# Performance work log

Hardware: AMD Instinct MI355X
Metric: run time of the kernel (lower is better)

Reference implementation:

```python
import math
import jax, jax.numpy as jnp
import numpy as np

HIDDEN = 2048
N_HEADS = 16
N_KV_HEADS = 4
HEAD_DIM = HIDDEN // N_HEADS  # 128
SEQ = 2048
BATCH = 2
RMS_EPS = 1.1920928955078125e-07  # torch float32 eps (nn.RMSNorm default eps=None)


def setup_inputs() -> dict:
    key = jax.random.key(0)
    ks = jax.random.split(key, 8)
    x = jax.random.normal(ks[0], (BATCH, SEQ, HIDDEN), dtype=jnp.float32)
    # RoPE tables, half-rotation layout: [f0..f_{d/2-1}, f0..f_{d/2-1}]
    inv_freq = 1.0 / (10000.0 ** (jnp.arange(0, HEAD_DIM, 2, dtype=jnp.float32) / HEAD_DIM))
    t = jnp.arange(SEQ, dtype=jnp.float32)
    freqs = jnp.outer(t, inv_freq)                      # [S, D/2]
    emb = jnp.concatenate([freqs, freqs], axis=-1)      # [S, D]
    sin, cos = jnp.sin(emb), jnp.cos(emb)
    s = 0.02
    Wq = jax.random.normal(ks[1], (HIDDEN, HIDDEN), dtype=jnp.float32) * s
    Wk = jax.random.normal(ks[2], (HIDDEN, N_KV_HEADS * HEAD_DIM), dtype=jnp.float32) * s
    Wv = jax.random.normal(ks[3], (HIDDEN, N_KV_HEADS * HEAD_DIM), dtype=jnp.float32) * s
    Wo = jax.random.normal(ks[4], (HIDDEN, HIDDEN), dtype=jnp.float32) * s
    q_norm_w = jnp.ones((HEAD_DIM,), dtype=jnp.float32)
    k_norm_w = jnp.ones((HEAD_DIM,), dtype=jnp.float32)
    return {"x": x, "sin": sin, "cos": cos, "Wq": Wq, "Wk": Wk, "Wv": Wv,
            "Wo": Wo, "q_norm_w": q_norm_w, "k_norm_w": k_norm_w}


def _rms_norm(t, w):
    # RMSNorm over last dim (head_dim) with learned weight
    var = jnp.mean(t * t, axis=-1, keepdims=True)
    return t * jax.lax.rsqrt(var + RMS_EPS) * w


def _apply_rope(t, sin, cos):
    # t: [B, H, S, D]; sin/cos: [S, D] broadcast
    half = t.shape[-1] // 2
    rotated = jnp.concatenate([-t[..., half:], t[..., :half]], axis=-1)
    return cos * t + sin * rotated


def reference(x, sin, cos, Wq, Wk, Wv, Wo, q_norm_w, k_norm_w):
    b, s, _ = x.shape
    rep = N_HEADS // N_KV_HEADS
    # Q: proj -> norm -> transpose -> rope
    q = (x @ Wq).reshape(b, s, N_HEADS, HEAD_DIM)
    q = _rms_norm(q, q_norm_w).transpose(0, 2, 1, 3)           # [B, H, S, D]
    q = _apply_rope(q, sin, cos)
    # K: proj -> repeat kv heads -> norm -> transpose -> rope
    k = (x @ Wk).reshape(b, s, N_KV_HEADS, HEAD_DIM)
    k = jnp.repeat(k, rep, axis=2)                              # [B, S, H, D]
    k = _rms_norm(k, k_norm_w).transpose(0, 2, 1, 3)            # [B, H, S, D]
    k = _apply_rope(k, sin, cos)
    # V: proj -> repeat kv heads -> transpose
    v = (x @ Wv).reshape(b, s, N_KV_HEADS, HEAD_DIM)
    v = jnp.repeat(v, rep, axis=2).transpose(0, 2, 1, 3)        # [B, H, S, D]
    # explicit masked softmax attention (materializes [B,H,S,S])
    scores = jnp.einsum('bhqd,bhkd->bhqk', q, k) / math.sqrt(HEAD_DIM)
    causal = jnp.triu(jnp.ones((s, s), dtype=bool), 1)
    scores = jnp.where(causal, -jnp.inf, scores)
    attn = jax.nn.softmax(scores, axis=-1)
    o = jnp.einsum('bhqk,bhkd->bhqd', attn, v)                  # [B, H, S, D]
    o = o.transpose(0, 2, 1, 3).reshape(b, s, HIDDEN)
    return o @ Wo
```

## Files before the change

kernel.cpp:

```cpp
#include <hip/hip_runtime.h>

typedef __attribute__((ext_vector_type(8))) short bf16x8;
typedef __attribute__((ext_vector_type(4))) short bf16x4;
typedef __attribute__((ext_vector_type(4))) float f32x4;

#define HIDDEN 2048
#define NH 16
#define NKV 4
#define HD 128
#define SEQ_N 2048
#define NT 4096
#define QKV_N 3072
#define RMS_EPS 1.1920928955078125e-07f
#define QSCALE 0.08838834764831845f
#define SM_C 12.0f

static __device__ __forceinline__ float b2f(unsigned short u) {
  union { unsigned int i; float f; } v; v.i = ((unsigned int)u) << 16; return v.f;
}
static __device__ __forceinline__ unsigned short f2b(float f) {
  union { float f; unsigned int i; } v; v.f = f;
  unsigned int r = (v.i + 0x7fffu + ((v.i >> 16) & 1u)) >> 16;
  return (unsigned short)r;
}
static __device__ __forceinline__ void gload_lds16(const unsigned short* g, unsigned short* l) {
  __builtin_amdgcn_global_load_lds(
      (const __attribute__((address_space(1))) unsigned int*)g,
      (__attribute__((address_space(3))) unsigned int*)l, 16, 0, 0);
}
static __device__ __forceinline__ void store_c(float* p, float v) { *p = v; }
static __device__ __forceinline__ void store_c(unsigned short* p, float v) { *p = f2b(v); }

template <typename OutT>
__device__ __forceinline__ void gemm_tile(
    const unsigned short* __restrict__ A, int lda,
    const unsigned short* __restrict__ BT, int ldb,
    OutT* __restrict__ C, int ldc,
    int K, int m0, int nloc0, int nout0) {
  __shared__ unsigned short As[4096], Bs[4096];
  const int tid  = threadIdx.x;
  const int wid  = tid >> 6, lane = tid & 63;
  const int g    = lane >> 4, cc = lane & 15;
  const int wr   = wid >> 1,  wc = wid & 1;
  const int r0   = tid >> 2;
  const int cb0  = (tid & 3) * 8;

  f32x4 acc[4][4];
#pragma unroll
  for (int i = 0; i < 4; ++i)
#pragma unroll
    for (int j = 0; j < 4; ++j) acc[i][j] = (f32x4){0.f, 0.f, 0.f, 0.f};

  unsigned short* AsW0 = As + wid * 512;
  unsigned short* AsW1 = As + 2048 + wid * 512;
  unsigned short* BsW0 = Bs + wid * 512;
  unsigned short* BsW1 = Bs + 2048 + wid * 512;
  const unsigned short* Ab0 = A  + (size_t)(m0 + r0)        * lda + cb0;
  const unsigned short* Ab1 = A  + (size_t)(m0 + 64 + r0)   * lda + cb0;
  const unsigned short* Bb0 = BT + (size_t)(nloc0 + r0)     * ldb + cb0;
  const unsigned short* Bb1 = BT + (size_t)(nloc0 + 64 + r0)* ldb + cb0;

  for (int kt = 0; kt < K; kt += 32) {
    gload_lds16(Ab0 + kt, AsW0);
    gload_lds16(Ab1 + kt, AsW1);
    gload_lds16(Bb0 + kt, BsW0);
    gload_lds16(Bb1 + kt, BsW1);
    __syncthreads();
    bf16x8 af[4], bfr[4];
#pragma unroll
    for (int mi = 0; mi < 4; ++mi)
      af[mi] = *(const bf16x8*)(As + ((wr * 64 + mi * 16 + cc) * 32 + g * 8));
#pragma unroll
    for (int ni = 0; ni < 4; ++ni)
      bfr[ni] = *(const bf16x8*)(Bs + ((wc * 64 + ni * 16 + cc) * 32 + g * 8));
#pragma unroll
    for (int mi = 0; mi < 4; ++mi)
#pragma unroll
      for (int ni = 0; ni < 4; ++ni)
        acc[mi][ni] = __builtin_amdgcn_mfma_f32_16x16x32_bf16(af[mi], bfr[ni], acc[mi][ni], 0, 0, 0);
    __syncthreads();
  }
#pragma unroll
  for (int mi = 0; mi < 4; ++mi)
#pragma unroll
    for (int ni = 0; ni < 4; ++ni)
#pragma unroll
      for (int j = 0; j < 4; ++j) {
        int row = m0 + wr * 64 + mi * 16 + g * 4 + j;
        int col = nout0 + wc * 64 + ni * 16 + cc;
        store_c(&C[(size_t)row * ldc + col], acc[mi][ni][j]);
      }
}

__global__ __launch_bounds__(256) void k_gemm_qkv(
    const unsigned short* __restrict__ x,
    const unsigned short* __restrict__ WqT,
    const unsigned short* __restrict__ WkT,
    const unsigned short* __restrict__ WvT,
    unsigned short* __restrict__ Praw) {
  int wg = (blockIdx.x & 7) * 96 + (blockIdx.x >> 3);
  int nb = wg % 24, mb = wg / 24;
  int n0 = nb * 128;
  const unsigned short* BT; int nloc;
  if (n0 < HIDDEN)            { BT = WqT; nloc = n0; }
  else if (n0 < HIDDEN + 512) { BT = WkT; nloc = n0 - HIDDEN; }
  else                        { BT = WvT; nloc = n0 - (HIDDEN + 512); }
  gemm_tile<unsigned short>(x, HIDDEN, BT, HIDDEN, Praw, QKV_N, HIDDEN, mb * 128, nloc, n0);
}

__global__ __launch_bounds__(256) void k_gemm_o(
    const unsigned short* __restrict__ Oa,
    const unsigned short* __restrict__ WoT,
    float* __restrict__ out) {
  int wg = (blockIdx.x & 7) * 64 + (blockIdx.x >> 3);
  int nb = wg % 16, mb = wg / 16;
  gemm_tile<float>(Oa, HIDDEN, WoT, HIDDEN, out, HIDDEN, HIDDEN, mb * 128, nb * 128, nb * 128);
}

__global__ __launch_bounds__(256) void k_cvt_f2b(
    const float* __restrict__ src, unsigned short* __restrict__ dst) {
  int i = (blockIdx.x * 256 + threadIdx.x) * 8;
  float4 a = *(const float4*)(src + i);
  float4 b = *(const float4*)(src + i + 4);
  bf16x8 v;
  v[0] = (short)f2b(a.x); v[1] = (short)f2b(a.y); v[2] = (short)f2b(a.z); v[3] = (short)f2b(a.w);
  v[4] = (short)f2b(b.x); v[5] = (short)f2b(b.y); v[6] = (short)f2b(b.z); v[7] = (short)f2b(b.w);
  *(bf16x8*)(dst + i) = v;
}

__global__ __launch_bounds__(256) void k_transpose_f2b(
    const float* __restrict__ src, unsigned short* __restrict__ dst,
    int ld_src, int ld_dst, int tilesC) {
  __shared__ float T[64][68];
  int tr = blockIdx.x / tilesC, tc = blockIdx.x % tilesC;
  int r0 = tr * 64, c0 = tc * 64;
  int tid = threadIdx.x;
#pragma unroll
  for (int it = 0; it < 4; ++it) {
    int u = it * 256 + tid;
    int r = u >> 4, cb = (u & 15) * 4;
    float4 v = *(const float4*)(src + (size_t)(r0 + r) * ld_src + c0 + cb);
    T[r][cb] = v.x; T[r][cb + 1] = v.y; T[r][cb + 2] = v.z; T[r][cb + 3] = v.w;
  }
  __syncthreads();
#pragma unroll
  for (int it = 0; it < 2; ++it) {
    int u = it * 256 + tid;
    int dc = u >> 3, rb = (u & 7) * 8;
    bf16x8 v;
#pragma unroll
    for (int j = 0; j < 8; ++j) v[j] = (short)f2b(T[rb + j][dc]);
    *(bf16x8*)(dst + (size_t)(c0 + dc) * ld_dst + r0 + rb) = v;
  }
}

__global__ __launch_bounds__(256) void k_transpose_bb(
    const unsigned short* __restrict__ src, unsigned short* __restrict__ dst,
    int ld_src, int ld_dst, int tilesC) {
  __shared__ unsigned short T[64][80];
  int tr = blockIdx.x / tilesC, tc = blockIdx.x % tilesC;
  int r0 = tr * 64, c0 = tc * 64;
  int tid = threadIdx.x;
#pragma unroll
  for (int it = 0; it < 2; ++it) {
    int u = it * 256 + tid; int r = u >> 3, cb = (u & 7) * 8;
    bf16x8 v = *(const bf16x8*)(src + (size_t)(r0 + r) * ld_src + c0 + cb);
    *(bf16x8*)(&T[r][cb]) = v;
  }
  __syncthreads();
#pragma unroll
  for (int it = 0; it < 2; ++it) {
    int u = it * 256 + tid; int dc = u >> 3, rb = (u & 7) * 8;
    bf16x8 v;
#pragma unroll
    for (int j = 0; j < 8; ++j) v[j] = (short)T[rb + j][dc];
    *(bf16x8*)(dst + (size_t)(c0 + dc) * ld_dst + r0 + rb) = v;
  }
}

__global__ __launch_bounds__(256) void k_qk_post(
    const unsigned short* __restrict__ Praw,
    const float* __restrict__ sinT,
    const float* __restrict__ cosT,
    const float* __restrict__ qw,
    const float* __restrict__ kw,
    unsigned short* __restrict__ Qbuf,
    unsigned short* __restrict__ Kbuf) {
  int sub = threadIdx.x >> 4;
  int sl  = threadIdx.x & 15;
  int rid = blockIdx.x * 16 + sub;
  int t = rid / 20, slot = rid - t * 20;
  int b = t >> 11, s = t & 2047;
  const int isq = (slot < 16);
  int cb = isq ? slot * 128 : HIDDEN + (slot - 16) * 128;
  const unsigned short* src = Praw + (size_t)t * QKV_N + cb;
  const int d0 = sl * 4;
  bf16x4 a0 = *(const bf16x4*)(src + d0);
  bf16x4 a1 = *(const bf16x4*)(src + 64 + d0);
  float x0[4], x1[4];
  float ssq = 0.f;
#pragma unroll
  for (int j = 0; j < 4; ++j) {
    x0[j] = b2f((unsigned short)a0[j]);
    x1[j] = b2f((unsigned short)a1[j]);
    ssq += x0[j] * x0[j] + x1[j] * x1[j];
  }
#pragma unroll
  for (int mk = 1; mk < 16; mk <<= 1) ssq += __shfl_xor(ssq, mk, 64);
  float r = rsqrtf(ssq * (1.0f / 128.0f) + RMS_EPS);
  const float* w = isq ? qw : kw;
  f32x4 w0 = *(const f32x4*)(w + d0);
  f32x4 w1 = *(const f32x4*)(w + 64 + d0);
  f32x4 cs0 = *(const f32x4*)(cosT + s * 128 + d0);
  f32x4 cs1 = *(const f32x4*)(cosT + s * 128 + 64 + d0);
  f32x4 sn0 = *(const f32x4*)(sinT + s * 128 + d0);
  f32x4 sn1 = *(const f32x4*)(sinT + s * 128 + 64 + d0);
  unsigned short* dst = isq
      ? Qbuf + ((size_t)(b * NH + slot) * SEQ_N + s) * HD
      : Kbuf + ((size_t)(b * NKV + (slot - 16)) * SEQ_N + s) * HD;
  const float qs = isq ? QSCALE : 1.0f;
  bf16x4 o0, o1;
#pragma unroll
  for (int j = 0; j < 4; ++j) {
    float n0 = x0[j] * r * w0[j];
    float n1 = x1[j] * r * w1[j];
    o0[j] = (short)f2b((cs0[j] * n0 - sn0[j] * n1) * qs);
    o1[j] = (short)f2b((cs1[j] * n1 + sn1[j] * n0) * qs);
  }
  *(bf16x4*)(dst + d0) = o0;
  *(bf16x4*)(dst + 64 + d0) = o1;
}

__global__ __launch_bounds__(256, 2) void k_attn(
    const unsigned short* __restrict__ Q,
    const unsigned short* __restrict__ K,
    const unsigned short* __restrict__ V,
    unsigned short* __restrict__ O) {
  __shared__ unsigned short Ks[2][64 * 128];
  __shared__ unsigned short Vs[2][128 * 64];
  __shared__ unsigned short Ps[4][16 * 64];
  const int tid = threadIdx.x, wid = tid >> 6, lane = tid & 63;
  const int g = lane >> 4, c = lane & 15;
  const int bid = blockIdx.x;
  const int bh = bid & 31;
  const int b = bh >> 4, h = bh & 15;
  const int z = bid >> 5;
  const int zz = z & 7, zr = z >> 3;
  const int qt = (zr == 0) ? zz : (zr == 1) ? 15 - zz : (zr == 2) ? 16 + zz : 31 - zz;
  const int wq0 = qt * 64 + wid * 16;
  const int kv = h >> 2;
  const int nt = qt + 1;

  const unsigned short* Qp = Q + (size_t)(b * NH + h) * SEQ_N * HD;
  const unsigned short* Kp = K + (size_t)(b * NKV + kv) * SEQ_N * HD;
  const unsigned short* Vp = V + (size_t)(kv * HD) * NT + b * SEQ_N;

  const int krow_l = lane >> 4;
  const int kcol_l = (lane & 15) * 8;
  const int vrow_l = lane >> 3;
  const int vcol_l = (lane & 7) * 8;

  bf16x8 qfr[4];
#pragma unroll
  for (int ks = 0; ks < 4; ++ks)
    qfr[ks] = *(const bf16x8*)(Qp + (size_t)(wq0 + c) * HD + ks * 32 + g * 8);

  f32x4 o[8];
#pragma unroll
  for (int df = 0; df < 8; ++df) o[df] = (f32x4){0.f, 0.f, 0.f, 0.f};
  float l_i[4] = {0.f, 0.f, 0.f, 0.f};

#define STAGE(BUF, KBASE)                                                          \
  {                                                                                \
    _Pragma("unroll")                                                              \
    for (int ch = 0; ch < 4; ++ch) {                                               \
      int chunk = wid * 4 + ch;                                                    \
      int rk = chunk * 4 + krow_l;                                                 \
      int ck = kcol_l ^ ((rk & 15) << 3);                                          \
      gload_lds16(Kp + (size_t)((KBASE) + rk) * HD + ck, &Ks[BUF][chunk * 512]);   \
      int rv = chunk * 8 + vrow_l;                                                 \
      int cv = vcol_l ^ ((rv & 7) << 3);                                           \
      gload_lds16(Vp + (size_t)rv * NT + (KBASE) + cv, &Vs[BUF][chunk * 512]);     \
    }                                                                              \
  }

  int buf = 0;
  STAGE(0, 0);
  __syncthreads();

  for (int kt = 0; kt < nt; ++kt) {
    const int kbase = kt * 64;
    if (kt + 1 < nt) STAGE(buf ^ 1, kbase + 64);

    f32x4 s[4];
#pragma unroll
    for (int kf = 0; kf < 4; ++kf) s[kf] = (f32x4){0.f, 0.f, 0.f, 0.f};
    __builtin_amdgcn_s_setprio(1);
#pragma unroll
    for (int ks = 0; ks < 4; ++ks) {
      bf16x8 bk[4];
#pragma unroll
      for (int kf = 0; kf < 4; ++kf) {
        int r = kf * 16 + c;
        int e = (ks * 32 + g * 8) ^ ((r & 15) << 3);
        bk[kf] = *(const bf16x8*)(&Ks[buf][r * 128 + e]);
      }
#pragma unroll
      for (int kf = 0; kf < 4; ++kf)
        s[kf] = __builtin_amdgcn_mfma_f32_16x16x32_bf16(qfr[ks], bk[kf], s[kf], 0, 0, 0);
    }
    __builtin_amdgcn_s_setprio(0);
    if (kbase + 63 > wq0) {
#pragma unroll
      for (int kf = 0; kf < 4; ++kf)
#pragma unroll
        for (int i = 0; i < 4; ++i) {
          int q = wq0 + g * 4 + i;
          int kp = kbase + kf * 16 + c;
          if (kp > q) s[kf][i] = -1e30f;
        }
    }
#pragma unroll
    for (int kf = 0; kf < 4; ++kf)
#pragma unroll
      for (int i = 0; i < 4; ++i) {
        float p = __expf(s[kf][i] - SM_C);
        l_i[i] += p;
        int r = g * 4 + i;
        int e = (kf * 16 + c) ^ ((r & 7) << 3);
        Ps[wid][r * 64 + e] = f2b(p);
      }
    __builtin_amdgcn_s_setprio(1);
#pragma unroll
    for (int ksp = 0; ksp < 2; ++ksp) {
      int ep = (ksp * 32 + g * 8) ^ ((c & 7) << 3);
      bf16x8 pa = *(const bf16x8*)(&Ps[wid][c * 64 + ep]);
#pragma unroll
      for (int df = 0; df < 8; ++df) {
        int rv = df * 16 + c;
        int e = (ksp * 32 + g * 8) ^ ((rv & 7) << 3);
        bf16x8 vb = *(const bf16x8*)(&Vs[buf][rv * 64 + e]);
        o[df] = __builtin_amdgcn_mfma_f32_16x16x32_bf16(pa, vb, o[df], 0, 0, 0);
      }
    }
    __builtin_amdgcn_s_setprio(0);
    __syncthreads();
    buf ^= 1;
  }

  unsigned short* Op = O + (size_t)(b * SEQ_N) * HIDDEN + h * HD;
#pragma unroll
  for (int i = 0; i < 4; ++i) {
    float t = l_i[i];
    t += __shfl_xor(t, 1, 64);
    t += __shfl_xor(t, 2, 64);
    t += __shfl_xor(t, 4, 64);
    t += __shfl_xor(t, 8, 64);
    float inv = 1.0f / t;
    int q = wq0 + g * 4 + i;
#pragma unroll
    for (int df = 0; df < 8; ++df)
      Op[(size_t)q * HIDDEN + df * 16 + c] = f2b(o[df][i] * inv);
  }
#undef STAGE
}

extern "C" void kernel_launch(void* const* d_in, const int* in_sizes, int n_in,
                              void* d_out, int out_size, void* d_ws, size_t ws_size,
                              hipStream_t stream) {
  const float* x    = (const float*)d_in[0];
  const float* sinT = (const float*)d_in[1];
  const float* cosT = (const float*)d_in[2];
  const float* Wq   = (const float*)d_in[3];
  const float* Wk   = (const float*)d_in[4];
  const float* Wv   = (const float*)d_in[5];
  const float* Wo   = (const float*)d_in[6];
  const float* qw   = (const float*)d_in[7];
  const float* kw   = (const float*)d_in[8];
  float* out = (float*)d_out;
  unsigned short* ws = (unsigned short*)d_ws;

  unsigned short* Xb   = ws;
  unsigned short* WqT  = ws + 8388608;
  unsigned short* WkT  = ws + 12582912;
  unsigned short* WvT  = ws + 13631488;
  unsigned short* WoT  = ws + 14680064;
  unsigned short* Praw = ws + 18874368;
  unsigned short* Qbuf = ws + 31457280;
  unsigned short* Kbuf = ws + 39845888;
  unsigned short* Vt   = ws + 41943040;
  unsigned short* Oatt = ws + 44040192;

  dim3 blk(256);
  k_cvt_f2b<<<4096, blk, 0, stream>>>(x, Xb);
  k_transpose_f2b<<<1024, blk, 0, stream>>>(Wq, WqT, 2048, 2048, 32);
  k_transpose_f2b<<<256,  blk, 0, stream>>>(Wk, WkT, 512,  2048, 8);
  k_transpose_f2b<<<256,  blk, 0, stream>>>(Wv, WvT, 512,  2048, 8);
  k_transpose_f2b<<<1024, blk, 0, stream>>>(Wo, WoT, 2048, 2048, 32);
  k_gemm_qkv<<<768, blk, 0, stream>>>(Xb, WqT, WkT, WvT, Praw);
  k_qk_post<<<5120, blk, 0, stream>>>(Praw, sinT, cosT, qw, kw, Qbuf, Kbuf);
  k_transpose_bb<<<512, blk, 0, stream>>>(Praw + 2560, Vt, 3072, 4096, 8);
  k_attn<<<1024, blk, 0, stream>>>(Qbuf, Kbuf, Vt, Oatt);
  k_gemm_o<<<512, blk, 0, stream>>>(Oatt, WoT, out);
}
```

Measured before the change: 321.0 us.

## Rewrite projection GEMMs with 128x256 tiles, double-buffered LDS and XOR swizzle

Replaces the single-buffered 128x128 GEMM tile (256 threads, K-step 32) with a 128x256 tile run by 512 threads that steps K by 64. The LDS is double-buffered so the next stage is prefetched while the current one is computed, using explicit vmcnt waits and raw barriers. Reads use an XOR swizzle to avoid bank conflicts, and MFMA sections are bracketed by s_setprio. This targets the per-iteration sync and load latency and raises data reuse, at the cost of much larger LDS use (96KB per block) and fewer blocks in the QKV and O GEMM grids.

```diff
diff --git a/kernel.cpp b/kernel.cpp
--- a/kernel.cpp
+++ b/kernel.cpp
@@ -32,18 +32,18 @@
 static __device__ __forceinline__ void store_c(unsigned short* p, float v) { *p = f2b(v); }
 
 template <typename OutT>
-__device__ __forceinline__ void gemm_tile(
+__device__ __forceinline__ void gemm8_tile(
     const unsigned short* __restrict__ A, int lda,
     const unsigned short* __restrict__ BT, int ldb,
     OutT* __restrict__ C, int ldc,
     int K, int m0, int nloc0, int nout0) {
-  __shared__ unsigned short As[4096], Bs[4096];
-  const int tid  = threadIdx.x;
-  const int wid  = tid >> 6, lane = tid & 63;
-  const int g    = lane >> 4, cc = lane & 15;
-  const int wr   = wid >> 1,  wc = wid & 1;
-  const int r0   = tid >> 2;
-  const int cb0  = (tid & 3) * 8;
+  __shared__ unsigned short As[2][128 * 64];
+  __shared__ unsigned short Bs[2][256 * 64];
+  const int tid = threadIdx.x;
+  const int wid = tid >> 6, lane = tid & 63;
+  const int g = lane >> 4, cc = lane & 15;
+  const int wr = wid >> 2, wc = wid & 3;
+  const int sr = lane >> 3, scb = lane & 7;
 
   f32x4 acc[4][4];
 #pragma unroll
@@ -51,35 +51,73 @@
 #pragma unroll
     for (int j = 0; j < 4; ++j) acc[i][j] = (f32x4){0.f, 0.f, 0.f, 0.f};
 
-  unsigned short* AsW0 = As + wid * 512;
-  unsigned short* AsW1 = As + 2048 + wid * 512;
-  unsigned short* BsW0 = Bs + wid * 512;
-  unsigned short* BsW1 = Bs + 2048 + wid * 512;
-  const unsigned short* Ab0 = A  + (size_t)(m0 + r0)        * lda + cb0;
-  const unsigned short* Ab1 = A  + (size_t)(m0 + 64 + r0)   * lda + cb0;
-  const unsigned short* Bb0 = BT + (size_t)(nloc0 + r0)     * ldb + cb0;
-  const unsigned short* Bb1 = BT + (size_t)(nloc0 + 64 + r0)* ldb + cb0;
-
-  for (int kt = 0; kt < K; kt += 32) {
-    gload_lds16(Ab0 + kt, AsW0);
-    gload_lds16(Ab1 + kt, AsW1);
-    gload_lds16(Bb0 + kt, BsW0);
-    gload_lds16(Bb1 + kt, BsW1);
-    __syncthreads();
-    bf16x8 af[4], bfr[4];
-#pragma unroll
-    for (int mi = 0; mi < 4; ++mi)
-      af[mi] = *(const bf16x8*)(As + ((wr * 64 + mi * 16 + cc) * 32 + g * 8));
+#define STAGE8(BUF, KT)                                                              \
+  {                                                                                  \
+    _Pragma("unroll")                                                                \
+    for (int i = 0; i < 2; ++i) {                                                    \
+      int r = i * 64 + wid * 8 + sr;                                                 \
+      gload_lds16(A + (size_t)(m0 + r) * lda + (KT) + ((scb ^ (r & 7)) << 3),        \
+                  &As[BUF][i * 4096 + wid * 512]);                                   \
+    }                                                                                \
+    _Pragma("unroll")                                                                \
+    for (int i = 0; i < 4; ++i) {                                                    \
+      int r = i * 64 + wid * 8 + sr;                                                 \
+      gload_lds16(BT + (size_t)(nloc0 + r) * ldb + (KT) + ((scb ^ (r & 7)) << 3),    \
+                  &Bs[BUF][i * 4096 + wid * 512]);                                   \
+    }                                                                                \
+  }
+
+  int buf = 0;
+  STAGE8(0, 0);
+  STAGE8(1, 64);
+  asm volatile("s_waitcnt vmcnt(6)" ::: "memory");
+  __builtin_amdgcn_s_barrier();
+  asm volatile("" ::: "memory");
+
+  for (int kt = 0; kt < K; kt += 64) {
+    bf16x8 bfr[4][2];
 #pragma unroll
     for (int ni = 0; ni < 4; ++ni)
-      bfr[ni] = *(const bf16x8*)(Bs + ((wc * 64 + ni * 16 + cc) * 32 + g * 8));
-#pragma unroll
-    for (int mi = 0; mi < 4; ++mi)
-#pragma unroll
-      for (int ni = 0; ni < 4; ++ni)
-        acc[mi][ni] = __builtin_amdgcn_mfma_f32_16x16x32_bf16(af[mi], bfr[ni], acc[mi][ni], 0, 0, 0);
-    __syncthreads();
-  }
+#pragma unroll
+      for (int ks = 0; ks < 2; ++ks) {
+        int row = wc * 64 + ni * 16 + cc;
+        bfr[ni][ks] = *(const bf16x8*)(&Bs[buf][row * 64 + (((ks * 4 + g) ^ (row & 7)) << 3)]);
+      }
+#pragma unroll
+    for (int mp = 0; mp < 2; ++mp) {
+      bf16x8 af[2][2];
+#pragma unroll
+      for (int mi = 0; mi < 2; ++mi)
+#pragma unroll
+        for (int ks = 0; ks < 2; ++ks) {
+          int row = wr * 64 + (mp * 2 + mi) * 16 + cc;
+          af[mi][ks] = *(const bf16x8*)(&As[buf][row * 64 + (((ks * 4 + g) ^ (row & 7)) << 3)]);
+        }
+      __builtin_amdgcn_s_setprio(1);
+#pragma unroll
+      for (int mi = 0; mi < 2; ++mi)
+#pragma unroll
+        for (int ni = 0; ni < 4; ++ni)
+#pragma unroll
+          for (int ks = 0; ks < 2; ++ks)
+            acc[mp * 2 + mi][ni] = __builtin_amdgcn_mfma_f32_16x16x32_bf16(
+                af[mi][ks], bfr[ni][ks], acc[mp * 2 + mi][ni], 0, 0, 0);
+      __builtin_amdgcn_s_setprio(0);
+    }
+    asm volatile("" ::: "memory");
+    __builtin_amdgcn_s_barrier();
+    asm volatile("" ::: "memory");
+    if (kt + 128 < K) {
+      STAGE8(buf, kt + 128);
+      asm volatile("s_waitcnt vmcnt(6)" ::: "memory");
+    } else {
+      asm volatile("s_waitcnt vmcnt(0)" ::: "memory");
+    }
+    __builtin_amdgcn_s_barrier();
+    asm volatile("" ::: "memory");
+    buf ^= 1;
+  }
+
 #pragma unroll
   for (int mi = 0; mi < 4; ++mi)
 #pragma unroll
@@ -90,31 +128,32 @@
         int col = nout0 + wc * 64 + ni * 16 + cc;
         store_c(&C[(size_t)row * ldc + col], acc[mi][ni][j]);
       }
-}
-
-__global__ __launch_bounds__(256) void k_gemm_qkv(
+#undef STAGE8
+}
+
+__global__ __launch_bounds__(512, 2) void k_gemm_qkv(
     const unsigned short* __restrict__ x,
     const unsigned short* __restrict__ WqT,
     const unsigned short* __restrict__ WkT,
     const unsigned short* __restrict__ WvT,
     unsigned short* __restrict__ Praw) {
-  int wg = (blockIdx.x & 7) * 96 + (blockIdx.x >> 3);
-  int nb = wg % 24, mb = wg / 24;
-  int n0 = nb * 128;
+  int wg = (blockIdx.x & 7) * 48 + (blockIdx.x >> 3);
+  int mb = wg & 31, nb = wg >> 5;
+  int n0 = nb * 256;
   const unsigned short* BT; int nloc;
   if (n0 < HIDDEN)            { BT = WqT; nloc = n0; }
   else if (n0 < HIDDEN + 512) { BT = WkT; nloc = n0 - HIDDEN; }
   else                        { BT = WvT; nloc = n0 - (HIDDEN + 512); }
-  gemm_tile<unsigned short>(x, HIDDEN, BT, HIDDEN, Praw, QKV_N, HIDDEN, mb * 128, nloc, n0);
-}
-
-__global__ __launch_bounds__(256) void k_gemm_o(
+  gemm8_tile<unsigned short>(x, HIDDEN, BT, HIDDEN, Praw, QKV_N, HIDDEN, mb * 128, nloc, n0);
+}
+
+__global__ __launch_bounds__(512, 2) void k_gemm_o(
     const unsigned short* __restrict__ Oa,
     const unsigned short* __restrict__ WoT,
     float* __restrict__ out) {
-  int wg = (blockIdx.x & 7) * 64 + (blockIdx.x >> 3);
-  int nb = wg % 16, mb = wg / 16;
-  gemm_tile<float>(Oa, HIDDEN, WoT, HIDDEN, out, HIDDEN, HIDDEN, mb * 128, nb * 128, nb * 128);
+  int wg = (blockIdx.x & 7) * 32 + (blockIdx.x >> 3);
+  int mb = wg & 31, nb = wg >> 5;
+  gemm8_tile<float>(Oa, HIDDEN, WoT, HIDDEN, out, HIDDEN, HIDDEN, mb * 128, nb * 256, nb * 256);
 }
 
 __global__ __launch_bounds__(256) void k_cvt_f2b(
@@ -397,9 +436,9 @@
   k_transpose_f2b<<<256,  blk, 0, stream>>>(Wk, WkT, 512,  2048, 8);
   k_transpose_f2b<<<256,  blk, 0, stream>>>(Wv, WvT, 512,  2048, 8);
   k_transpose_f2b<<<1024, blk, 0, stream>>>(Wo, WoT, 2048, 2048, 32);
-  k_gemm_qkv<<<768, blk, 0, stream>>>(Xb, WqT, WkT, WvT, Praw);
+  k_gemm_qkv<<<384, dim3(512), 0, stream>>>(Xb, WqT, WkT, WvT, Praw);
   k_qk_post<<<5120, blk, 0, stream>>>(Praw, sinT, cosT, qw, kw, Qbuf, Kbuf);
   k_transpose_bb<<<512, blk, 0, stream>>>(Praw + 2560, Vt, 3072, 4096, 8);
   k_attn<<<1024, blk, 0, stream>>>(Qbuf, Kbuf, Vt, Oatt);
-  k_gemm_o<<<512, blk, 0, stream>>>(Oatt, WoT, out);
-}
+  k_gemm_o<<<256, dim3(512), 0, stream>>>(Oatt, WoT, out);
+}
```

After: 353.5 us. +10.1%, slower.
